# Kernel tuning notes

Measured on AMD Instinct MI355X. Metric: run time of the kernel, lower is better.

The kernel has to match this reference:

```python
import jax, jax.numpy as jnp
import numpy as np

H = 16      # num_heads
D = 1024    # hidden_dim
HD = D // H # head_dim = 64


def setup_inputs() -> dict:
    key = jax.random.key(0)
    ks = jax.random.split(key, 9)
    s = 1.0 / np.sqrt(D)
    return {
        "hidden_states": jax.random.normal(ks[0], (2, 2048, D), dtype=jnp.float32),
        "wq": jax.random.uniform(ks[1], (D, D), jnp.float32, -s, s),
        "bq": jax.random.uniform(ks[2], (D,), jnp.float32, -s, s),
        "wk": jax.random.uniform(ks[3], (D, D), jnp.float32, -s, s),
        "bk": jax.random.uniform(ks[4], (D,), jnp.float32, -s, s),
        "wv": jax.random.uniform(ks[5], (D, D), jnp.float32, -s, s),
        "bv": jax.random.uniform(ks[6], (D,), jnp.float32, -s, s),
        "wo": jax.random.uniform(ks[7], (D, D), jnp.float32, -s, s),
        "bo": jax.random.uniform(ks[8], (D,), jnp.float32, -s, s),
    }


def reference(hidden_states, wq, bq, wk, bk, wv, bv, wo, bo):
    B, L, _ = hidden_states.shape
    scale = HD ** -0.5
    # projections: [B,L,D] -> [B,H,L,HD]
    def split_heads(x):
        return x.reshape(B, L, H, HD).transpose(0, 2, 1, 3)
    q = split_heads(hidden_states @ wq.T + bq)
    k = split_heads(hidden_states @ wk.T + bk)
    v = split_heads(hidden_states @ wv.T + bv)
    # explicit [B,H,L,L] scores + softmax + weighted sum (faithful to source)
    scores = jnp.einsum("bhqd,bhkd->bhqk", q, k) * scale
    attn = jax.nn.softmax(scores, axis=-1)
    out = jnp.einsum("bhqk,bhkd->bhqd", attn, v)
    out = out.transpose(0, 2, 1, 3).reshape(B, L, D)
    return out @ wo.T + bo
```

## Files before the change

### kernel.cpp

```cpp
#include <hip/hip_runtime.h>
#include <math.h>

#define BATCH  2
#define SEQ    2048
#define NH     16
#define DMODEL 1024
#define DHEAD  64

typedef short short8 __attribute__((ext_vector_type(8)));
typedef float f32x4 __attribute__((ext_vector_type(4)));

#define QSCALE 0.18033688011112042f

__device__ __forceinline__ ushort f2bf(float f) {
  unsigned int u = __builtin_bit_cast(unsigned int, f);
  u = (u + 0x7FFFu + ((u >> 16) & 1u)) >> 16;
  return (ushort)u;
}

__device__ __forceinline__ unsigned int cvtpk(float lo, float hi) {
  unsigned int r;
  asm("v_cvt_pk_bf16_f32 %0, %1, %2" : "=v"(r) : "v"(lo), "v"(hi));
  return r;
}

__global__ __launch_bounds__(256) void cast_all(
    const float* __restrict__ hs, const float* __restrict__ wq,
    const float* __restrict__ wk, const float* __restrict__ wv,
    const float* __restrict__ wo,
    ushort* __restrict__ hsb, ushort* __restrict__ wqb,
    ushort* __restrict__ wkb, ushort* __restrict__ wvb,
    ushort* __restrict__ wob) {
  const int z = blockIdx.y;
  const float* s = (z == 0) ? hs : (z == 1) ? wq : (z == 2) ? wk
                   : (z == 3) ? wv : wo;
  ushort* d = (z == 0) ? hsb : (z == 1) ? wqb : (z == 2) ? wkb
              : (z == 3) ? wvb : wob;
  const int n = (z == 0) ? BATCH * SEQ * DMODEL : DMODEL * DMODEL;
  const int i = (blockIdx.x * 256 + threadIdx.x) * 8;
  if (i < n) {
    const float4 a = *(const float4*)(s + i);
    const float4 b = *(const float4*)(s + i + 4);
    short8 o;
    o[0] = (short)f2bf(a.x); o[1] = (short)f2bf(a.y);
    o[2] = (short)f2bf(a.z); o[3] = (short)f2bf(a.w);
    o[4] = (short)f2bf(b.x); o[5] = (short)f2bf(b.y);
    o[6] = (short)f2bf(b.z); o[7] = (short)f2bf(b.w);
    *(short8*)(d + i) = o;
  }
}

__device__ __forceinline__ void mfma_gemm_core(
    const ushort* __restrict__ X, const ushort* __restrict__ W,
    f32x4 (&acc)[4][2]) {
  __shared__ ushort Al[128][40];
  __shared__ ushort Bl[128][40];
  const int tid = threadIdx.x;
  const int lane = tid & 63;
  const int w8 = tid >> 6;
  const int wm = w8 >> 2;
  const int wn = w8 & 3;
  const int m16 = lane & 15;
  const int g4 = lane >> 4;
  const int m0 = blockIdx.y << 7;
  const int n0 = blockIdx.x << 7;

  const int srow = tid >> 2;
  const int sseg = (tid & 3) << 3;
  const ushort* ap = X + (size_t)(m0 + srow) * DMODEL + sseg;
  const ushort* wp = W + (size_t)(n0 + srow) * DMODEL + sseg;

  short8 pa = *(const short8*)(ap);
  short8 pb = *(const short8*)(wp);

  for (int kt = 0; kt < DMODEL / 32; ++kt) {
    __syncthreads();
    *(short8*)&Al[srow][sseg] = pa;
    *(short8*)&Bl[srow][sseg] = pb;
    __syncthreads();
    if (kt < DMODEL / 32 - 1) {
      pa = *(const short8*)(ap + (kt + 1) * 32);
      pb = *(const short8*)(wp + (kt + 1) * 32);
    }
    short8 af[4], bf[2];
#pragma unroll
    for (int mi = 0; mi < 4; ++mi)
      af[mi] = *(const short8*)&Al[(wm << 6) + (mi << 4) + m16][g4 << 3];
#pragma unroll
    for (int ni = 0; ni < 2; ++ni)
      bf[ni] = *(const short8*)&Bl[(wn << 5) + (ni << 4) + m16][g4 << 3];
#pragma unroll
    for (int mi = 0; mi < 4; ++mi)
#pragma unroll
      for (int ni = 0; ni < 2; ++ni)
        acc[mi][ni] = __builtin_amdgcn_mfma_f32_16x16x32_bf16(
            af[mi], bf[ni], acc[mi][ni], 0, 0, 0);
  }
}

__global__ __launch_bounds__(512) void qkv_mfma(
    const ushort* __restrict__ X,
    const ushort* __restrict__ wqb, const ushort* __restrict__ wkb,
    const ushort* __restrict__ wvb,
    const float* __restrict__ bq, const float* __restrict__ bk,
    const float* __restrict__ bv,
    ushort* __restrict__ Qb, ushort* __restrict__ Kb,
    ushort* __restrict__ Vb) {
  const int z = blockIdx.z;
  const ushort* W = (z == 0) ? wqb : (z == 1) ? wkb : wvb;
  const float* bias = (z == 0) ? bq : (z == 1) ? bk : bv;
  ushort* Y = (z == 0) ? Qb : (z == 1) ? Kb : Vb;
  const float oscale = (z == 0) ? QSCALE : 1.0f;

  f32x4 acc[4][2];
#pragma unroll
  for (int mi = 0; mi < 4; ++mi)
#pragma unroll
    for (int ni = 0; ni < 2; ++ni) acc[mi][ni] = (f32x4){0.f, 0.f, 0.f, 0.f};
  mfma_gemm_core(X, W, acc);

  const int tid = threadIdx.x;
  const int lane = tid & 63;
  const int w8 = tid >> 6;
  const int wm = w8 >> 2, wn = w8 & 3;
  const int m16 = lane & 15, g4 = lane >> 4;
  const int m0 = blockIdx.y << 7, n0 = blockIdx.x << 7;
#pragma unroll
  for (int ni = 0; ni < 2; ++ni) {
    const int col = n0 + (wn << 5) + (ni << 4) + m16;
    const float bv4 = bias[col];
#pragma unroll
    for (int mi = 0; mi < 4; ++mi)
#pragma unroll
      for (int r = 0; r < 4; ++r) {
        const int row = m0 + (wm << 6) + (mi << 4) + (g4 << 2) + r;
        Y[(size_t)row * DMODEL + col] = f2bf((acc[mi][ni][r] + bv4) * oscale);
      }
  }
}

__global__ __launch_bounds__(512) void oproj_mfma(
    const ushort* __restrict__ X, const ushort* __restrict__ wob,
    const float* __restrict__ bo, float* __restrict__ Y) {
  f32x4 acc[4][2];
#pragma unroll
  for (int mi = 0; mi < 4; ++mi)
#pragma unroll
    for (int ni = 0; ni < 2; ++ni) acc[mi][ni] = (f32x4){0.f, 0.f, 0.f, 0.f};
  mfma_gemm_core(X, wob, acc);

  const int tid = threadIdx.x;
  const int lane = tid & 63;
  const int w8 = tid >> 6;
  const int wm = w8 >> 2, wn = w8 & 3;
  const int m16 = lane & 15, g4 = lane >> 4;
  const int m0 = blockIdx.y << 7, n0 = blockIdx.x << 7;
#pragma unroll
  for (int ni = 0; ni < 2; ++ni) {
    const int col = n0 + (wn << 5) + (ni << 4) + m16;
    const float bv4 = bo[col];
#pragma unroll
    for (int mi = 0; mi < 4; ++mi)
#pragma unroll
      for (int r = 0; r < 4; ++r) {
        const int row = m0 + (wm << 6) + (mi << 4) + (g4 << 2) + r;
        Y[(size_t)row * DMODEL + col] = acc[mi][ni][r] + bv4;
      }
  }
}

__global__ __launch_bounds__(256, 2) void attn_mfma(
    const ushort* __restrict__ Q, const ushort* __restrict__ K,
    const ushort* __restrict__ V, ushort* __restrict__ O) {
  __shared__ ushort Klds[2][64][72];
  __shared__ ushort Vlds[2][64][72];
  __shared__ ushort Plds[4][32][72];

  const int tid = threadIdx.x;
  const int lane = tid & 63;
  const int wv = tid >> 6;
  const int m16 = lane & 15;
  const int g4 = lane >> 4;
  const int b = blockIdx.z;
  const int h = blockIdx.y;
  const int q0 = (blockIdx.x << 7) + (wv << 5);

  const size_t base = ((size_t)b * SEQ) * DMODEL + h * DHEAD;

  short8 qf[2][2];
#pragma unroll
  for (int qh = 0; qh < 2; ++qh) {
    const ushort* qp =
        Q + base + (size_t)(q0 + (qh << 4) + m16) * DMODEL + (g4 << 3);
    qf[qh][0] = *(const short8*)(qp);
    qf[qh][1] = *(const short8*)(qp + 32);
  }

  f32x4 oacc[2][4];
#pragma unroll
  for (int qh = 0; qh < 2; ++qh)
#pragma unroll
    for (int dt = 0; dt < 4; ++dt) oacc[qh][dt] = (f32x4){0.f, 0.f, 0.f, 0.f};
  float mrow[2] = {-1e30f, -1e30f};
  float lsum[2] = {0.f, 0.f};

  const int skey = tid >> 2;
  const int sb = tid & 3;
  const ushort* kgp = K + base + (size_t)skey * DMODEL + (sb << 3);
  const ushort* vgp = V + base + (size_t)skey * DMODEL + (sb << 3);
  const int vsw0 = skey ^ (sb << 3);
  const int vsw1 = skey ^ ((sb + 4) << 3);

  short8 kv0 = *(const short8*)(kgp);
  short8 kv1 = *(const short8*)(kgp + 32);
  short8 vv0 = *(const short8*)(vgp);
  short8 vv1 = *(const short8*)(vgp + 32);

  int p = 0;
  for (int kt = 0; kt < SEQ / 64; ++kt) {
    *(short8*)&Klds[p][skey][sb << 3] = kv0;
    *(short8*)&Klds[p][skey][(sb + 4) << 3] = kv1;
#pragma unroll
    for (int i = 0; i < 8; ++i) {
      Vlds[p][(sb << 3) + i][vsw0] = ((const ushort*)&vv0)[i];
      Vlds[p][((sb + 4) << 3) + i][vsw1] = ((const ushort*)&vv1)[i];
    }
    __syncthreads();
    if (kt + 1 < SEQ / 64) {
      const size_t koff = (size_t)(kt + 1) * 64 * DMODEL;
      kv0 = *(const short8*)(kgp + koff);
      kv1 = *(const short8*)(kgp + koff + 32);
      vv0 = *(const short8*)(vgp + koff);
      vv1 = *(const short8*)(vgp + koff + 32);
    }

    f32x4 s[2][4];
#pragma unroll
    for (int qh = 0; qh < 2; ++qh)
#pragma unroll
      for (int kt2 = 0; kt2 < 4; ++kt2) s[qh][kt2] = (f32x4){0.f, 0.f, 0.f, 0.f};
    __builtin_amdgcn_s_setprio(1);
#pragma unroll
    for (int ks = 0; ks < 2; ++ks) {
#pragma unroll
      for (int kt2 = 0; kt2 < 4; ++kt2) {
        const short8 kf =
            *(const short8*)&Klds[p][(kt2 << 4) + m16][(ks << 5) + (g4 << 3)];
        s[0][kt2] =
            __builtin_amdgcn_mfma_f32_16x16x32_bf16(kf, qf[0][ks], s[0][kt2], 0, 0, 0);
        s[1][kt2] =
            __builtin_amdgcn_mfma_f32_16x16x32_bf16(kf, qf[1][ks], s[1][kt2], 0, 0, 0);
      }
    }
    __builtin_amdgcn_s_setprio(0);

#pragma unroll
    for (int qh = 0; qh < 2; ++qh) {
      float t0 = fmaxf(fmaxf(s[qh][0][0], s[qh][0][1]),
                       fmaxf(s[qh][0][2], s[qh][0][3]));
      float t1 = fmaxf(fmaxf(s[qh][1][0], s[qh][1][1]),
                       fmaxf(s[qh][1][2], s[qh][1][3]));
      float t2 = fmaxf(fmaxf(s[qh][2][0], s[qh][2][1]),
                       fmaxf(s[qh][2][2], s[qh][2][3]));
      float t3 = fmaxf(fmaxf(s[qh][3][0], s[qh][3][1]),
                       fmaxf(s[qh][3][2], s[qh][3][3]));
      float tred = fmaxf(fmaxf(t0, t1), fmaxf(t2, t3));
      tred = fmaxf(tred, __shfl_xor(tred, 16));
      tred = fmaxf(tred, __shfl_xor(tred, 32));
      if (!__all(tred <= mrow[qh] + 8.0f)) {
        const float mnew = fmaxf(mrow[qh], tred);
        const float corr = exp2f(mrow[qh] - mnew);
        lsum[qh] *= corr;
        const float cb0 = __shfl(corr, (g4 << 2) + 0);
        const float cb1 = __shfl(corr, (g4 << 2) + 1);
        const float cb2 = __shfl(corr, (g4 << 2) + 2);
        const float cb3 = __shfl(corr, (g4 << 2) + 3);
#pragma unroll
        for (int dt = 0; dt < 4; ++dt) {
          oacc[qh][dt][0] *= cb0; oacc[qh][dt][1] *= cb1;
          oacc[qh][dt][2] *= cb2; oacc[qh][dt][3] *= cb3;
        }
        mrow[qh] = mnew;
      }
      float ps = 0.f;
#pragma unroll
      for (int kt2 = 0; kt2 < 4; ++kt2)
#pragma unroll
        for (int r = 0; r < 4; ++r) {
          const float pv = exp2f(s[qh][kt2][r] - mrow[qh]);
          s[qh][kt2][r] = pv;
          ps += pv;
        }
      lsum[qh] += ps;
#pragma unroll
      for (int kt2 = 0; kt2 < 4; ++kt2) {
        const unsigned int lo = cvtpk(s[qh][kt2][0], s[qh][kt2][1]);
        const unsigned int hi = cvtpk(s[qh][kt2][2], s[qh][kt2][3]);
        uint2* dst =
            (uint2*)&Plds[wv][(qh << 4) + m16][(kt2 << 4) + (g4 << 2)];
        *dst = make_uint2(lo, hi);
      }
    }

    short8 pf[2][2];
#pragma unroll
    for (int qh = 0; qh < 2; ++qh)
#pragma unroll
      for (int ks = 0; ks < 2; ++ks)
        pf[qh][ks] =
            *(const short8*)&Plds[wv][(qh << 4) + m16][(ks << 5) + (g4 << 3)];
    __builtin_amdgcn_s_setprio(1);
#pragma unroll
    for (int dt = 0; dt < 4; ++dt) {
      const int d = (dt << 4) + m16;
      const int swz = (d >> 3) << 3;
#pragma unroll
      for (int ks = 0; ks < 2; ++ks) {
        const short8 vf =
            *(const short8*)&Vlds[p][d][((ks << 5) + (g4 << 3)) ^ swz];
        oacc[0][dt] =
            __builtin_amdgcn_mfma_f32_16x16x32_bf16(pf[0][ks], vf, oacc[0][dt], 0, 0, 0);
        oacc[1][dt] =
            __builtin_amdgcn_mfma_f32_16x16x32_bf16(pf[1][ks], vf, oacc[1][dt], 0, 0, 0);
      }
    }
    __builtin_amdgcn_s_setprio(0);
    p ^= 1;
  }

#pragma unroll
  for (int qh = 0; qh < 2; ++qh) {
    float ls = lsum[qh];
    ls += __shfl_xor(ls, 16);
    ls += __shfl_xor(ls, 32);
    const float inv = 1.0f / ls;
    const float inv0 = __shfl(inv, (g4 << 2) + 0);
    const float inv1 = __shfl(inv, (g4 << 2) + 1);
    const float inv2 = __shfl(inv, (g4 << 2) + 2);
    const float inv3 = __shfl(inv, (g4 << 2) + 3);
    const float invr[4] = {inv0, inv1, inv2, inv3};
#pragma unroll
    for (int r = 0; r < 4; ++r) {
      const size_t row = (size_t)(q0 + (qh << 4) + (g4 << 2) + r);
      ushort* op = O + ((size_t)b * SEQ + row) * DMODEL + h * DHEAD + m16;
#pragma unroll
      for (int dt = 0; dt < 4; ++dt)
        op[dt << 4] = f2bf(oacc[qh][dt][r] * invr[r]);
    }
  }
}

extern "C" void kernel_launch(void* const* d_in, const int* in_sizes, int n_in,
                              void* d_out, int out_size, void* d_ws,
                              size_t ws_size, hipStream_t stream) {
  const float* hs = (const float*)d_in[0];
  const float* wq = (const float*)d_in[1];
  const float* bq = (const float*)d_in[2];
  const float* wk = (const float*)d_in[3];
  const float* bk = (const float*)d_in[4];
  const float* wv = (const float*)d_in[5];
  const float* bv = (const float*)d_in[6];
  const float* wo = (const float*)d_in[7];
  const float* bo = (const float*)d_in[8];
  float* out = (float*)d_out;

  const size_t elems = (size_t)BATCH * SEQ * DMODEL;
  const size_t welems = (size_t)DMODEL * DMODEL;
  ushort* hsb = (ushort*)d_ws;
  ushort* wqb = hsb + elems;
  ushort* wkb = wqb + welems;
  ushort* wvb = wkb + welems;
  ushort* wob = wvb + welems;
  ushort* Qb = wob + welems;
  ushort* Kb = Qb + elems;
  ushort* Vb = Kb + elems;
  ushort* Ab = Vb + elems;

  cast_all<<<dim3((int)(elems / (256 * 8)), 5, 1), 256, 0, stream>>>(
      hs, wq, wk, wv, wo, hsb, wqb, wkb, wvb, wob);
  qkv_mfma<<<dim3(DMODEL / 128, (BATCH * SEQ) / 128, 3), 512, 0, stream>>>(
      hsb, wqb, wkb, wvb, bq, bk, bv, Qb, Kb, Vb);
  attn_mfma<<<dim3(SEQ / 128, NH, BATCH), 256, 0, stream>>>(Qb, Kb, Vb, Ab);
  oproj_mfma<<<dim3(DMODEL / 128, (BATCH * SEQ) / 128, 1), 512, 0, stream>>>(
      Ab, wob, bo, out);
}
```

Measured before the change: 148.2 us.

## Transpose P tile in registers via lane shuffles instead of LDS round-trip

Replaces the per-wave LDS staging of the softmax probability tile with cross-lane shuffle swaps, so the P fragments feed the PV MFMA without LDS writes and reads. It also drops the Plds shared buffer and raises launch bounds to 4 blocks per SM to increase occupancy. The tradeoff is extra shuffle and select instructions, plus possible register pressure from the tighter register budget implied by the higher occupancy target. The key reordering is also an implicit permutation of the k dimension, which must match the V fragment layout.

```diff
diff --git a/kernel.cpp b/kernel.cpp
--- a/kernel.cpp
+++ b/kernel.cpp
@@ -169,12 +169,19 @@
   }
 }
 
-__global__ __launch_bounds__(256, 2) void attn_mfma(
+#define SWAPSTEP(Wa, Wb, dist, hi)                  \
+  {                                                 \
+    const unsigned int gv = (hi) ? (Wa) : (Wb);     \
+    const unsigned int gt = __shfl_xor(gv, (dist)); \
+    (Wa) = (hi) ? gt : (Wa);                        \
+    (Wb) = (hi) ? (Wb) : gt;                        \
+  }
+
+__global__ __launch_bounds__(256, 4) void attn_mfma(
     const ushort* __restrict__ Q, const ushort* __restrict__ K,
     const ushort* __restrict__ V, ushort* __restrict__ O) {
   __shared__ ushort Klds[2][64][72];
   __shared__ ushort Vlds[2][64][72];
-  __shared__ ushort Plds[4][32][72];
 
   const int tid = threadIdx.x;
   const int lane = tid & 63;
@@ -238,7 +245,8 @@
 #pragma unroll
     for (int qh = 0; qh < 2; ++qh)
 #pragma unroll
-      for (int kt2 = 0; kt2 < 4; ++kt2) s[qh][kt2] = (f32x4){0.f, 0.f, 0.f, 0.f};
+      for (int kt2 = 0; kt2 < 4; ++kt2)
+        s[qh][kt2] = (f32x4){0.f, 0.f, 0.f, 0.f};
     __builtin_amdgcn_s_setprio(1);
 #pragma unroll
     for (int ks = 0; ks < 2; ++ks) {
@@ -246,14 +254,15 @@
       for (int kt2 = 0; kt2 < 4; ++kt2) {
         const short8 kf =
             *(const short8*)&Klds[p][(kt2 << 4) + m16][(ks << 5) + (g4 << 3)];
-        s[0][kt2] =
-            __builtin_amdgcn_mfma_f32_16x16x32_bf16(kf, qf[0][ks], s[0][kt2], 0, 0, 0);
-        s[1][kt2] =
-            __builtin_amdgcn_mfma_f32_16x16x32_bf16(kf, qf[1][ks], s[1][kt2], 0, 0, 0);
+        s[0][kt2] = __builtin_amdgcn_mfma_f32_16x16x32_bf16(
+            kf, qf[0][ks], s[0][kt2], 0, 0, 0);
+        s[1][kt2] = __builtin_amdgcn_mfma_f32_16x16x32_bf16(
+            kf, qf[1][ks], s[1][kt2], 0, 0, 0);
       }
     }
     __builtin_amdgcn_s_setprio(0);
 
+    short8 pk[2][2];
 #pragma unroll
     for (int qh = 0; qh < 2; ++qh) {
       float t0 = fmaxf(fmaxf(s[qh][0][0], s[qh][0][1]),
@@ -292,37 +301,51 @@
           ps += pv;
         }
       lsum[qh] += ps;
-#pragma unroll
-      for (int kt2 = 0; kt2 < 4; ++kt2) {
-        const unsigned int lo = cvtpk(s[qh][kt2][0], s[qh][kt2][1]);
-        const unsigned int hi = cvtpk(s[qh][kt2][2], s[qh][kt2][3]);
-        uint2* dst =
-            (uint2*)&Plds[wv][(qh << 4) + m16][(kt2 << 4) + (g4 << 2)];
-        *dst = make_uint2(lo, hi);
-      }
-    }
-
-    short8 pf[2][2];
-#pragma unroll
-    for (int qh = 0; qh < 2; ++qh)
-#pragma unroll
-      for (int ks = 0; ks < 2; ++ks)
-        pf[qh][ks] =
-            *(const short8*)&Plds[wv][(qh << 4) + m16][(ks << 5) + (g4 << 3)];
+
+      unsigned int W0 = cvtpk(s[qh][0][0], s[qh][0][1]);
+      unsigned int W1 = cvtpk(s[qh][0][2], s[qh][0][3]);
+      unsigned int W2 = cvtpk(s[qh][1][0], s[qh][1][1]);
+      unsigned int W3 = cvtpk(s[qh][1][2], s[qh][1][3]);
+      unsigned int W4 = cvtpk(s[qh][2][0], s[qh][2][1]);
+      unsigned int W5 = cvtpk(s[qh][2][2], s[qh][2][3]);
+      unsigned int W6 = cvtpk(s[qh][3][0], s[qh][3][1]);
+      unsigned int W7 = cvtpk(s[qh][3][2], s[qh][3][3]);
+      {
+        const bool hi = (lane & 32) != 0;
+        SWAPSTEP(W0, W2, 32, hi);
+        SWAPSTEP(W1, W3, 32, hi);
+        SWAPSTEP(W4, W6, 32, hi);
+        SWAPSTEP(W5, W7, 32, hi);
+      }
+      {
+        const bool hi = (lane & 16) != 0;
+        SWAPSTEP(W0, W2, 16, hi);
+        SWAPSTEP(W1, W3, 16, hi);
+        SWAPSTEP(W4, W6, 16, hi);
+        SWAPSTEP(W5, W7, 16, hi);
+      }
+      union { unsigned int u[4]; short8 v; } u0, u1;
+      u0.u[0] = W0; u0.u[1] = W1; u0.u[2] = W2; u0.u[3] = W3;
+      u1.u[0] = W4; u1.u[1] = W5; u1.u[2] = W6; u1.u[3] = W7;
+      pk[qh][0] = u0.v;
+      pk[qh][1] = u1.v;
+    }
+
     __builtin_amdgcn_s_setprio(1);
 #pragma unroll
     for (int dt = 0; dt < 4; ++dt) {
       const int d = (dt << 4) + m16;
       const int swz = (d >> 3) << 3;
-#pragma unroll
-      for (int ks = 0; ks < 2; ++ks) {
-        const short8 vf =
-            *(const short8*)&Vlds[p][d][((ks << 5) + (g4 << 3)) ^ swz];
-        oacc[0][dt] =
-            __builtin_amdgcn_mfma_f32_16x16x32_bf16(pf[0][ks], vf, oacc[0][dt], 0, 0, 0);
-        oacc[1][dt] =
-            __builtin_amdgcn_mfma_f32_16x16x32_bf16(pf[1][ks], vf, oacc[1][dt], 0, 0, 0);
-      }
+      const short8 vf0 = *(const short8*)&Vlds[p][d][(g4 << 3) ^ swz];
+      oacc[0][dt] = __builtin_amdgcn_mfma_f32_16x16x32_bf16(
+          pk[0][0], vf0, oacc[0][dt], 0, 0, 0);
+      oacc[1][dt] = __builtin_amdgcn_mfma_f32_16x16x32_bf16(
+          pk[1][0], vf0, oacc[1][dt], 0, 0, 0);
+      const short8 vf1 = *(const short8*)&Vlds[p][d][(32 + (g4 << 3)) ^ swz];
+      oacc[0][dt] = __builtin_amdgcn_mfma_f32_16x16x32_bf16(
+          pk[0][1], vf1, oacc[0][dt], 0, 0, 0);
+      oacc[1][dt] = __builtin_amdgcn_mfma_f32_16x16x32_bf16(
+          pk[1][1], vf1, oacc[1][dt], 0, 0, 0);
     }
     __builtin_amdgcn_s_setprio(0);
     p ^= 1;
```

Measured after the change: 164.4 us. 1.11x slower.
